# Optimization experiments

Measured on AMD Instinct MI355X. Metric: run time of the kernel, lower is better.

Reference implementation:

```python
import jax, jax.numpy as jnp
import numpy as np

ND, NP_, ED, EP, B = 8192, 8192, 262144, 262144, 4096
DIM = 300 + 1024 + 1024 + 1024  # 3372
EPS = 1e-5


def _bn(x, g, b):
    # BatchNorm1d in training mode: biased batch statistics
    m = x.mean(0)
    v = x.var(0)
    return (x - m) * jax.lax.rsqrt(v + EPS) * g + b


def _gcn(x, ei, ew, W, bias):
    # PyG GCNConv: add self-loops (weight 1), symmetric deg^-1/2 normalization,
    # linear transform, scatter-add aggregation at target nodes.
    N = x.shape[0]
    loop = jnp.arange(N)
    src = jnp.concatenate([ei[0], loop])
    dst = jnp.concatenate([ei[1], loop])
    w = jnp.concatenate([ew, jnp.ones((N,), ew.dtype)])
    deg = jax.ops.segment_sum(w, dst, num_segments=N)
    dinv = jnp.where(deg > 0, jax.lax.rsqrt(deg), 0.0)
    norm = dinv[src] * w * dinv[dst]          # [E+N]
    h = x @ W                                  # [N, 512]
    out = jax.ops.segment_sum(h[src] * norm[:, None], dst, num_segments=N) + bias
    return jax.nn.leaky_relu(out, 0.01)


def setup_inputs() -> dict:
    key = jax.random.key(0)
    ks = jax.random.split(key, 32)
    s = 0.02
    inp = {
        'd_index': jax.random.randint(ks[0], (B,), 0, ND),
        'p_index': jax.random.randint(ks[1], (B,), 0, NP_),
        'd_vecs': jax.random.normal(ks[2], (B, 300), jnp.float32),
        'p_embeddings': jax.random.normal(ks[3], (B, 1024), jnp.float32),
        'd_ecfps': jax.random.uniform(ks[4], (ND, 1024), jnp.float32),
        'd_ei': jax.random.randint(ks[5], (2, ED), 0, ND),
        'd_ew': jax.random.uniform(ks[6], (ED,), jnp.float32),
        'p_gos': jax.random.uniform(ks[7], (NP_, 1024), jnp.float32),
        'p_ei': jax.random.randint(ks[8], (2, EP), 0, NP_),
        'p_ew': jax.random.uniform(ks[9], (EP,), jnp.float32),
        'affinity': jax.random.uniform(ks[10], (ND, NP_), jnp.float32),
        # GCNConv params
        'W_e': jax.random.normal(ks[11], (1024, 512), jnp.float32) * s,
        'b_e': jnp.zeros((512,), jnp.float32),
        'W_g': jax.random.normal(ks[12], (1024, 512), jnp.float32) * s,
        'b_g': jnp.zeros((512,), jnp.float32),
        # lin1 / lin2
        'W1': jax.random.normal(ks[13], (512, 512), jnp.float32) * s,
        'b1': jnp.zeros((512,), jnp.float32),
        'W2': jax.random.normal(ks[14], (512, 512), jnp.float32) * s,
        'b2': jnp.zeros((512,), jnp.float32),
        # output MLP: 3372 -> 1024 -> 256 -> 1 with BN+ReLU (dropout = eval identity)
        'Wo1': jax.random.normal(ks[15], (DIM, 1024), jnp.float32) * s,
        'bo1': jnp.zeros((1024,), jnp.float32),
        'g1': jnp.ones((1024,), jnp.float32),
        'be1': jnp.zeros((1024,), jnp.float32),
        'Wo2': jax.random.normal(ks[16], (1024, 256), jnp.float32) * s,
        'bo2': jnp.zeros((256,), jnp.float32),
        'g2': jnp.ones((256,), jnp.float32),
        'be2': jnp.zeros((256,), jnp.float32),
        'Wo3': jax.random.normal(ks[17], (256, 1), jnp.float32) * s,
        'bo3': jnp.zeros((1,), jnp.float32),
    }
    return inp


def reference(d_index, p_index, d_vecs, p_embeddings, d_ecfps, d_ei, d_ew,
              p_gos, p_ei, p_ew, affinity,
              W_e, b_e, W_g, b_g, W1, b1, W2, b2,
              Wo1, bo1, g1, be1, Wo2, bo2, g2, be2, Wo3, bo3):
    ecfps = _gcn(d_ecfps, d_ei, d_ew, W_e, b_e)          # [ND, 512]
    gos = _gcn(p_gos, p_ei, p_ew, W_g, b_g)              # [NP, 512]
    drug = ecfps[d_index]                                 # [B, 512]
    protein = gos[p_index]                                # [B, 512]
    p2d = jax.nn.relu((affinity @ gos) @ W1 + b1)[d_index]      # [B, 512]
    d2p = jax.nn.relu((affinity.T @ ecfps) @ W2 + b2)[p_index]  # [B, 512]
    drug = jnp.concatenate([drug, p2d], axis=1)
    protein = jnp.concatenate([protein, d2p], axis=1)
    feature = jnp.concatenate([d_vecs, p_embeddings, drug, protein], axis=1)  # [B, 3372]
    h = jax.nn.relu(_bn(feature @ Wo1 + bo1, g1, be1))
    h = jax.nn.relu(_bn(h @ Wo2 + bo2, g2, be2))
    y = h @ Wo3 + bo3                                     # [B, 1]
    return y
```

## Files before the change

kernel.cpp:

```cpp
#include <hip/hip_runtime.h>
#include <stdint.h>
#include <stddef.h>

typedef unsigned short u16;
typedef unsigned int u32;
typedef __attribute__((ext_vector_type(8))) short bf16x8;
typedef __attribute__((ext_vector_type(8))) u16 u16x8;
typedef __attribute__((ext_vector_type(4))) float f32x4;

#define NDN 8192
#define NPN 8192
#define EDN 262144
#define EPN 262144
#define BBN 4096
#define KPAD 3392

__device__ __forceinline__ u16 f2b(float f) {
  u32 u = __float_as_uint(f);
  u32 r = (u + 0x7fffu + ((u >> 16) & 1u)) >> 16;
  return (u16)r;
}
__device__ __forceinline__ float b2f(u16 h) {
  return __uint_as_float(((u32)h) << 16);
}

__device__ __forceinline__ void gld_lds16(const void* g, void* l) {
  __builtin_amdgcn_global_load_lds(
      (const __attribute__((address_space(1))) u32*)g,
      (__attribute__((address_space(3))) u32*)l, 16, 0, 0);
}

template<int BM, int BN, int WM, int WN, bool GATHER>
__global__ void __launch_bounds__(256, 3)
gemm_bf16(const u16* __restrict__ A, int lda,
          const u16* __restrict__ Bt, int ldb,
          int N, int K, int KZ,
          const int* __restrict__ idx,
          float* __restrict__ Cf, u16* __restrict__ Cb, long zstride,
          const float* __restrict__ bias,
          const float* __restrict__ rowscale,
          int relu)
{
  constexpr int AISS = BM / 32;
  constexpr int BISS = BN / 32;
  constexpr int AF = WM / 16;
  constexpr int BF = WN / 16;
  constexpr int WGN = BN / WN;
  __shared__ __align__(16) u16 ldsA[BM * 64];
  __shared__ __align__(16) u16 ldsB[BN * 64];
  const int t = threadIdx.x;
  const int lane = t & 63;
  const int w = t >> 6;
  const int m0 = blockIdx.x * BM;
  const int n0 = blockIdx.y * BN;
  const int kOff = blockIdx.z * KZ;
  const int Kloc = min(KZ, K - kOff);
  const int wm = w / WGN, wn = w % WGN;
  const int sr = t >> 3;
  const int sk = (t & 7) * 8;

  if (zstride) Cf += (long)blockIdx.z * zstride;

  const u16* arow[AISS];
#pragma unroll
  for (int j = 0; j < AISS; ++j) {
    int r = m0 + j * 32 + sr;
    long rr = GATHER ? (long)idx[r] : (long)r;
    arow[j] = A + rr * (long)lda + sk + kOff;
  }
  const u16* brow[BISS];
#pragma unroll
  for (int j = 0; j < BISS; ++j)
    brow[j] = Bt + (long)(n0 + j * 32 + sr) * ldb + sk + kOff;

  f32x4 acc[AF][BF];
#pragma unroll
  for (int i = 0; i < AF; ++i)
#pragma unroll
    for (int j = 0; j < BF; ++j)
      acc[i][j] = (f32x4){0.f, 0.f, 0.f, 0.f};

  for (int k0 = 0; k0 < Kloc; k0 += 64) {
#pragma unroll
    for (int j = 0; j < AISS; ++j)
      gld_lds16(arow[j] + k0, &ldsA[(j * 32 + w * 8) * 64]);
#pragma unroll
    for (int j = 0; j < BISS; ++j)
      gld_lds16(brow[j] + k0, &ldsB[(j * 32 + w * 8) * 64]);
    __syncthreads();
#pragma unroll
    for (int k2 = 0; k2 < 64; k2 += 32) {
      bf16x8 af[AF], bfv[BF];
#pragma unroll
      for (int i = 0; i < AF; ++i)
        af[i] = *(const bf16x8*)&ldsA[(wm * WM + i * 16 + (lane & 15)) * 64 + k2 + (lane >> 4) * 8];
#pragma unroll
      for (int i = 0; i < BF; ++i)
        bfv[i] = *(const bf16x8*)&ldsB[(wn * WN + i * 16 + (lane & 15)) * 64 + k2 + (lane >> 4) * 8];
#pragma unroll
      for (int i = 0; i < AF; ++i)
#pragma unroll
        for (int j = 0; j < BF; ++j)
          acc[i][j] = __builtin_amdgcn_mfma_f32_16x16x32_bf16(af[i], bfv[j], acc[i][j], 0, 0, 0);
    }
    __syncthreads();
  }

  const int er = (lane >> 4) * 4;
  const int ecn = lane & 15;
#pragma unroll
  for (int i = 0; i < AF; ++i)
#pragma unroll
    for (int j = 0; j < BF; ++j)
#pragma unroll
      for (int r = 0; r < 4; ++r) {
        long gm = m0 + wm * WM + i * 16 + er + r;
        long gn = n0 + wn * WN + j * 16 + ecn;
        float v = acc[i][j][r];
        if (bias) v += bias[gn];
        if (rowscale) v *= rowscale[gm];
        if (relu) v = fmaxf(v, 0.f);
        if (Cb) Cb[gm * N + gn] = f2b(v);
        else    Cf[gm * N + gn] = v;
      }
}

__global__ void __launch_bounds__(256, 3)
gemm_a32g(const float* __restrict__ A, int lda,
          const u16* __restrict__ Bt, int ldb,
          int N, int KZ,
          const int* __restrict__ idx,
          float* __restrict__ Cf, long zstride)
{
  constexpr int AF = 2, BF = 8, WGN = 2;
  __shared__ __align__(16) u16 ldsA[64 * 72];
  __shared__ __align__(16) u16 ldsB[256 * 64];
  const int t = threadIdx.x;
  const int lane = t & 63;
  const int w = t >> 6;
  const int m0 = blockIdx.x * 64;
  const int n0 = blockIdx.y * 256;
  const int kOff = blockIdx.z * KZ;
  const int wm = w / WGN, wn = w % WGN;
  const int sr = t >> 3;
  const int sk = (t & 7) * 8;

  Cf += (long)blockIdx.z * zstride;

  const u16* brow[8];
#pragma unroll
  for (int j = 0; j < 8; ++j)
    brow[j] = Bt + (long)(n0 + j * 32 + sr) * ldb + sk + kOff;

  int r = m0 + (t >> 2);
  long rowsel = idx ? (long)idx[r] : (long)r;
  const float* ar_direct = A + rowsel * (long)lda + (t & 3) * 16 + kOff;

  f32x4 acc[AF][BF];
#pragma unroll
  for (int i = 0; i < AF; ++i)
#pragma unroll
    for (int j = 0; j < BF; ++j)
      acc[i][j] = (f32x4){0.f, 0.f, 0.f, 0.f};

  for (int k0 = 0; k0 < KZ; k0 += 64) {
#pragma unroll
    for (int j = 0; j < 8; ++j)
      gld_lds16(brow[j] + k0, &ldsB[(j * 32 + w * 8) * 64]);

    const float4* src = (const float4*)(ar_direct + k0);
    float4 v0 = src[0], v1 = src[1], v2 = src[2], v3 = src[3];
    u16x8 ua, ub;
    ua[0] = f2b(v0.x); ua[1] = f2b(v0.y); ua[2] = f2b(v0.z); ua[3] = f2b(v0.w);
    ua[4] = f2b(v1.x); ua[5] = f2b(v1.y); ua[6] = f2b(v1.z); ua[7] = f2b(v1.w);
    ub[0] = f2b(v2.x); ub[1] = f2b(v2.y); ub[2] = f2b(v2.z); ub[3] = f2b(v2.w);
    ub[4] = f2b(v3.x); ub[5] = f2b(v3.y); ub[6] = f2b(v3.z); ub[7] = f2b(v3.w);
    int ro = (t >> 2) * 72 + (t & 3) * 16;
    *(u16x8*)&ldsA[ro] = ua;
    *(u16x8*)&ldsA[ro + 8] = ub;
    __syncthreads();
#pragma unroll
    for (int k2 = 0; k2 < 64; k2 += 32) {
      bf16x8 af[AF], bfv[BF];
#pragma unroll
      for (int i = 0; i < AF; ++i)
        af[i] = *(const bf16x8*)&ldsA[(wm * 32 + i * 16 + (lane & 15)) * 72 + k2 + (lane >> 4) * 8];
#pragma unroll
      for (int i = 0; i < BF; ++i)
        bfv[i] = *(const bf16x8*)&ldsB[(wn * 128 + i * 16 + (lane & 15)) * 64 + k2 + (lane >> 4) * 8];
#pragma unroll
      for (int i = 0; i < AF; ++i)
#pragma unroll
        for (int j = 0; j < BF; ++j)
          acc[i][j] = __builtin_amdgcn_mfma_f32_16x16x32_bf16(af[i], bfv[j], acc[i][j], 0, 0, 0);
    }
    __syncthreads();
  }

  const int er = (lane >> 4) * 4;
  const int ecn = lane & 15;
#pragma unroll
  for (int i = 0; i < AF; ++i)
#pragma unroll
    for (int j = 0; j < BF; ++j)
#pragma unroll
      for (int rr2 = 0; rr2 < 4; ++rr2) {
        long gm = m0 + wm * 32 + i * 16 + er + rr2;
        long gn = n0 + wn * 128 + j * 16 + ecn;
        Cf[gm * N + gn] = acc[i][j][rr2];
      }
}

__global__ void reduceP(const float* __restrict__ p, long n, int parts,
                        int nmask, const float* __restrict__ bias,
                        float* __restrict__ out) {
  long i = ((long)blockIdx.x * 256 + threadIdx.x) * 4;
  if (i >= n) return;
  float4 a = *(const float4*)&p[i];
  for (int z = 1; z < parts; ++z) {
    float4 b = *(const float4*)&p[(long)z * n + i];
    a.x += b.x; a.y += b.y; a.z += b.z; a.w += b.w;
  }
  if (bias) {
    int c = (int)(i & nmask);
    a.x += bias[c]; a.y += bias[c + 1]; a.z += bias[c + 2]; a.w += bias[c + 3];
  }
  *(float4*)&out[i] = a;
}

__global__ void __launch_bounds__(256)
transcvt(const float* __restrict__ in, u16* __restrict__ out) {
  __shared__ float tile[64][65];
  const int t = threadIdx.x;
  const int r0 = blockIdx.x * 64, c0 = blockIdx.y * 64;
  {
    int rr = t >> 2, cb = (t & 3) * 16;
    const float4* src = (const float4*)&in[(long)(r0 + rr) * 8192 + c0 + cb];
    float4 a = src[0], b = src[1], c = src[2], d = src[3];
    float* dst = &tile[rr][cb];
    *(float4*)(dst) = a; *(float4*)(dst + 4) = b;
    *(float4*)(dst + 8) = c; *(float4*)(dst + 12) = d;
  }
  __syncthreads();
  {
    int cc = t >> 2, rb = (t & 3) * 16;
    u16x8 ua, ub;
#pragma unroll
    for (int j = 0; j < 8; ++j) {
      ua[j] = f2b(tile[rb + j][cc]);
      ub[j] = f2b(tile[rb + 8 + j][cc]);
    }
    u16* dst = &out[(long)(c0 + cc) * 8192 + r0 + rb];
    *(u16x8*)dst = ua;
    *(u16x8*)(dst + 8) = ub;
  }
}

__global__ void __launch_bounds__(256, 2)
gemm_sp(const float* __restrict__ A, int lda,
        const u16* __restrict__ Bt, int ldb,
        int N, int K,
        const float* __restrict__ bias,
        float* __restrict__ Cf)
{
  __shared__ __align__(16) u16 ldsAh[64 * 64];
  __shared__ __align__(16) u16 ldsAl[64 * 64];
  __shared__ __align__(16) u16 ldsB[64 * 64];
  const int t = threadIdx.x, lane = t & 63, w = t >> 6;
  const int m0 = blockIdx.x * 64, n0 = blockIdx.y * 64;
  const int wm = w >> 1, wn = w & 1;
  const int sr = t >> 3, sk = (t & 7) * 8;
  const int ar = t >> 2;
  const int ak = (t & 3) * 16;
  const float* Ap = A + (long)(m0 + ar) * lda + ak;
  const u16* brow[2];
#pragma unroll
  for (int j = 0; j < 2; ++j)
    brow[j] = Bt + (long)(n0 + j * 32 + sr) * ldb + sk;

  f32x4 acc[2][2];
#pragma unroll
  for (int i = 0; i < 2; ++i)
#pragma unroll
    for (int j = 0; j < 2; ++j)
      acc[i][j] = (f32x4){0.f, 0.f, 0.f, 0.f};

  for (int k0 = 0; k0 < K; k0 += 64) {
#pragma unroll
    for (int j = 0; j < 2; ++j)
      gld_lds16(brow[j] + k0, &ldsB[(j * 32 + w * 8) * 64]);
    const float4* src = (const float4*)(Ap + k0);
    float4 v0 = src[0], v1 = src[1], v2 = src[2], v3 = src[3];
    float f[16] = {v0.x, v0.y, v0.z, v0.w, v1.x, v1.y, v1.z, v1.w,
                   v2.x, v2.y, v2.z, v2.w, v3.x, v3.y, v3.z, v3.w};
    u16x8 h0, h1v, l0, l1v;
#pragma unroll
    for (int i = 0; i < 8; ++i) {
      u16 h = f2b(f[i]);       h0[i] = h;  l0[i] = f2b(f[i] - b2f(h));
      u16 g = f2b(f[8 + i]);   h1v[i] = g; l1v[i] = f2b(f[8 + i] - b2f(g));
    }
    *(u16x8*)&ldsAh[ar * 64 + ak] = h0;
    *(u16x8*)&ldsAh[ar * 64 + ak + 8] = h1v;
    *(u16x8*)&ldsAl[ar * 64 + ak] = l0;
    *(u16x8*)&ldsAl[ar * 64 + ak + 8] = l1v;
    __syncthreads();
#pragma unroll
    for (int k2 = 0; k2 < 64; k2 += 32) {
      bf16x8 ah[2], al[2], bv[2];
#pragma unroll
      for (int i = 0; i < 2; ++i) {
        int off = (wm * 32 + i * 16 + (lane & 15)) * 64 + k2 + (lane >> 4) * 8;
        ah[i] = *(const bf16x8*)&ldsAh[off];
        al[i] = *(const bf16x8*)&ldsAl[off];
      }
#pragma unroll
      for (int i = 0; i < 2; ++i)
        bv[i] = *(const bf16x8*)&ldsB[(wn * 32 + i * 16 + (lane & 15)) * 64 + k2 + (lane >> 4) * 8];
#pragma unroll
      for (int i = 0; i < 2; ++i)
#pragma unroll
        for (int j = 0; j < 2; ++j) {
          acc[i][j] = __builtin_amdgcn_mfma_f32_16x16x32_bf16(ah[i], bv[j], acc[i][j], 0, 0, 0);
          acc[i][j] = __builtin_amdgcn_mfma_f32_16x16x32_bf16(al[i], bv[j], acc[i][j], 0, 0, 0);
        }
    }
    __syncthreads();
  }

  const int er = (lane >> 4) * 4;
  const int ecn = lane & 15;
#pragma unroll
  for (int i = 0; i < 2; ++i)
#pragma unroll
    for (int j = 0; j < 2; ++j)
#pragma unroll
      for (int r = 0; r < 4; ++r) {
        long gm = m0 + wm * 32 + i * 16 + er + r;
        long gn = n0 + wn * 32 + j * 16 + ecn;
        float v = acc[i][j][r] + bias[gn];
        Cf[gm * N + gn] = fmaxf(v, 0.f);
      }
}

__global__ void cvt_bf16(const float* __restrict__ x, u16* __restrict__ y, long n) {
  long i = ((long)blockIdx.x * 256 + threadIdx.x) * 4;
  if (i < n) {
    float4 v = *(const float4*)&x[i];
    u16 a = f2b(v.x), b = f2b(v.y), c = f2b(v.z), d = f2b(v.w);
    u32 lo = (u32)a | ((u32)b << 16);
    u32 hi = (u32)c | ((u32)d << 16);
    *(uint2*)&y[i] = make_uint2(lo, hi);
  }
}

__global__ void wtrans(const float* __restrict__ in, u16* __restrict__ out,
                       int R, int C, int Rpad) {
  __shared__ float tile[32][33];
  int r0 = blockIdx.x * 32, c0 = blockIdx.y * 32;
  int tx = threadIdx.x & 31, ty = threadIdx.x >> 5;
  for (int j = 0; j < 32; j += 8) {
    int r = r0 + ty + j, c = c0 + tx;
    tile[ty + j][tx] = (r < R && c < C) ? in[(long)r * C + c] : 0.f;
  }
  __syncthreads();
  for (int j = 0; j < 32; j += 8) {
    int c = c0 + ty + j, r = r0 + tx;
    if (c < C && r < Rpad) out[(long)c * Rpad + r] = f2b(tile[tx][ty + j]);
  }
}

__global__ void btrans(const u16* __restrict__ in, u16* __restrict__ out, int R, int C) {
  __shared__ u16 tile[32][34];
  int r0 = blockIdx.x * 32, c0 = blockIdx.y * 32;
  int tx = threadIdx.x & 31, ty = threadIdx.x >> 5;
  for (int j = 0; j < 32; j += 8)
    tile[ty + j][tx] = in[(long)(r0 + ty + j) * C + c0 + tx];
  __syncthreads();
  for (int j = 0; j < 32; j += 8)
    out[(long)(c0 + ty + j) * R + r0 + tx] = tile[tx][ty + j];
}

__global__ void edge_deg2(const int* __restrict__ ei_a, const float* __restrict__ ew_a,
                          const int* __restrict__ ei_b, const float* __restrict__ ew_b,
                          int E, float* degw_a, int* cnt_a,
                          float* degw_b, int* cnt_b) {
  int e = blockIdx.x * 256 + threadIdx.x;
  if (e >= E) return;
  const int* ei = blockIdx.y ? ei_b : ei_a;
  const float* ew = blockIdx.y ? ew_b : ew_a;
  float* degw = blockIdx.y ? degw_b : degw_a;
  int* cnt = blockIdx.y ? cnt_b : cnt_a;
  int dst = ei[E + e];
  atomicAdd(&degw[dst], ew[e]);
  atomicAdd(&cnt[dst], 1);
}

__global__ void scan_dinv(const int* __restrict__ cnt_a, int* rowptr_a, int* cursor_a,
                          const float* __restrict__ degw_a, float* dinv_a,
                          const int* __restrict__ cnt_b, int* rowptr_b, int* cursor_b,
                          const float* __restrict__ degw_b, float* dinv_b) {
  const int* cnt = blockIdx.x ? cnt_b : cnt_a;
  int* rowptr = blockIdx.x ? rowptr_b : rowptr_a;
  int* cursor = blockIdx.x ? cursor_b : cursor_a;
  const float* degw = blockIdx.x ? degw_b : degw_a;
  float* dinv = blockIdx.x ? dinv_b : dinv_a;
  __shared__ int lds[256];
  int t = threadIdx.x;
  int c0 = t * 32;
  int loc[32];
  int s = 0;
#pragma unroll
  for (int i = 0; i < 32; ++i) { loc[i] = cnt[c0 + i]; s += loc[i]; }
  lds[t] = s;
  __syncthreads();
  for (int off = 1; off < 256; off <<= 1) {
    int add = (t >= off) ? lds[t - off] : 0;
    __syncthreads();
    lds[t] += add;
    __syncthreads();
  }
  int run = lds[t] - s;
#pragma unroll
  for (int i = 0; i < 32; ++i) {
    rowptr[c0 + i] = run;
    cursor[c0 + i] = run;
    run += loc[i];
  }
  if (t == 255) rowptr[8192] = run;
#pragma unroll
  for (int i = 0; i < 32; ++i)
    dinv[c0 + i] = rsqrtf(degw[c0 + i] + 1.0f);
}

__global__ void edge_scatter2(const int* __restrict__ ei_a, const float* __restrict__ ew_a,
                              const int* __restrict__ ei_b, const float* __restrict__ ew_b,
                              int E, int* cursor_a, int2* edges_a,
                              int* cursor_b, int2* edges_b) {
  int e = blockIdx.x * 256 + threadIdx.x;
  if (e >= E) return;
  const int* ei = blockIdx.y ? ei_b : ei_a;
  const float* ew = blockIdx.y ? ew_b : ew_a;
  int* cursor = blockIdx.y ? cursor_b : cursor_a;
  int2* edges = blockIdx.y ? edges_b : edges_a;
  int src = ei[e], dst = ei[E + e];
  int pos = atomicAdd(&cursor[dst], 1);
  edges[pos] = make_int2(src, __float_as_int(ew[e]));
}

__global__ void gcn_aggregate(const u16* __restrict__ hs,
                              const int* __restrict__ rowptr,
                              const int2* __restrict__ edges,
                              const float* __restrict__ dinv,
                              const float* __restrict__ bias,
                              u16* __restrict__ out) {
  const int i = blockIdx.x;
  const int t = threadIdx.x;
  const u32* base = (const u32*)hs;
  u32 hv = base[i * 256 + t];
  float a0 = b2f((u16)(hv & 0xffff));
  float a1 = b2f((u16)(hv >> 16));
  int s = rowptr[i], e = rowptr[i + 1];
  int p = s;
  for (; p + 4 <= e; p += 4) {
    int2 e0 = edges[p], e1 = edges[p + 1], e2 = edges[p + 2], e3 = edges[p + 3];
    u32 v0 = base[(long)e0.x * 256 + t];
    u32 v1 = base[(long)e1.x * 256 + t];
    u32 v2 = base[(long)e2.x * 256 + t];
    u32 v3 = base[(long)e3.x * 256 + t];
    float w0 = __int_as_float(e0.y), w1 = __int_as_float(e1.y);
    float w2 = __int_as_float(e2.y), w3 = __int_as_float(e3.y);
    a0 += w0 * b2f((u16)(v0 & 0xffff)); a1 += w0 * b2f((u16)(v0 >> 16));
    a0 += w1 * b2f((u16)(v1 & 0xffff)); a1 += w1 * b2f((u16)(v1 >> 16));
    a0 += w2 * b2f((u16)(v2 & 0xffff)); a1 += w2 * b2f((u16)(v2 >> 16));
    a0 += w3 * b2f((u16)(v3 & 0xffff)); a1 += w3 * b2f((u16)(v3 >> 16));
  }
  for (; p < e; ++p) {
    int2 ee = edges[p];
    u32 v = base[(long)ee.x * 256 + t];
    float ww = __int_as_float(ee.y);
    a0 += ww * b2f((u16)(v & 0xffff));
    a1 += ww * b2f((u16)(v >> 16));
  }
  float di = dinv[i];
  float o0 = bias[2 * t] + di * a0;
  float o1 = bias[2 * t + 1] + di * a1;
  o0 = (o0 >= 0.f) ? o0 : 0.01f * o0;
  o1 = (o1 >= 0.f) ? o1 : 0.01f * o1;
  ((u32*)out)[i * 256 + t] = (u32)f2b(o0) | ((u32)f2b(o1) << 16);
}

__global__ void colsum_all(const float* __restrict__ d_vecs, const float* __restrict__ p_emb,
                           const u16* __restrict__ ec, const u16* __restrict__ gos,
                           const float* __restrict__ t1, const float* __restrict__ t2,
                           const int* __restrict__ didx, const int* __restrict__ pidx,
                           float* __restrict__ out) {
  int c = blockIdx.x * 256 + threadIdx.x;
  if (c >= 3372) return;
  int r0 = blockIdx.y * 128;
  float s = 0.f;
  if (c < 300) {
    for (int r = r0; r < r0 + 128; ++r) s += d_vecs[(long)r * 300 + c];
  } else if (c < 1324) {
    int cc = c - 300;
    for (int r = r0; r < r0 + 128; ++r) s += p_emb[(long)r * 1024 + cc];
  } else if (c < 1836) {
    int cc = c - 1324;
    for (int r = r0; r < r0 + 128; ++r) s += b2f(ec[(long)didx[r] * 512 + cc]);
  } else if (c < 2348) {
    int cc = c - 1836;
    for (int r = r0; r < r0 + 128; ++r) s += t1[(long)r * 512 + cc];
  } else if (c < 2860) {
    int cc = c - 2348;
    for (int r = r0; r < r0 + 128; ++r) s += b2f(gos[(long)pidx[r] * 512 + cc]);
  } else {
    int cc = c - 2860;
    for (int r = r0; r < r0 + 128; ++r) s += t2[(long)r * 512 + cc];
  }
  atomicAdd(&out[c], s);
}

__global__ void assemble(const float* __restrict__ d_vecs, const float* __restrict__ p_emb,
                         const u16* __restrict__ ec, const u16* __restrict__ gos,
                         const float* __restrict__ t1, const float* __restrict__ t2,
                         const int* __restrict__ didx, const int* __restrict__ pidx,
                         const float* __restrict__ cs, u16* __restrict__ feat) {
  const float is = 1.f / 4096.f;
  int b = blockIdx.x;
  int t = threadIdx.x;
  long ob = (long)b * KPAD;
  int di = didx[b], pi = pidx[b];
  for (int j = t; j < 300; j += 256)
    feat[ob + j] = f2b(d_vecs[(long)b * 300 + j] - cs[j] * is);
  for (int j = t; j < 1024; j += 256)
    feat[ob + 300 + j] = f2b(p_emb[(long)b * 1024 + j] - cs[300 + j] * is);
  for (int j = t; j < 512; j += 256) {
    feat[ob + 1324 + j] = f2b(b2f(ec[(long)di * 512 + j]) - cs[1324 + j] * is);
    feat[ob + 1836 + j] = f2b(t1[(long)b * 512 + j] - cs[1836 + j] * is);
    feat[ob + 2348 + j] = f2b(b2f(gos[(long)pi * 512 + j]) - cs[2348 + j] * is);
    feat[ob + 2860 + j] = f2b(t2[(long)b * 512 + j] - cs[2860 + j] * is);
  }
  for (int j = t; j < 20; j += 256) feat[ob + 3372 + j] = 0;
}

__global__ void bn_stats(const float* __restrict__ x, int N,
                         float* __restrict__ sum, float* __restrict__ sumsq) {
  int r0 = blockIdx.x * 32;
  int t = threadIdx.x;
  for (int c = t; c < N; c += 256) {
    float s = 0.f, q = 0.f;
    for (int r = 0; r < 32; ++r) {
      float v = x[(long)(r0 + r) * N + c];
      s += v; q += v * v;
    }
    atomicAdd(&sum[c], s);
    atomicAdd(&sumsq[c], q);
  }
}

__global__ void bn_apply(const float* __restrict__ x, int M, int N, int nmask,
                         const float* __restrict__ sum, const float* __restrict__ sumsq,
                         const float* __restrict__ g, const float* __restrict__ be,
                         u16* __restrict__ y) {
  long i = (long)blockIdx.x * 256 + threadIdx.x;
  if (i >= (long)M * N) return;
  int c = (int)(i & nmask);
  float m = sum[c] / (float)M;
  float v = sumsq[c] / (float)M - m * m;
  float sc = g[c] * rsqrtf(v + 1e-5f);
  float sh = be[c] - m * sc;
  float o = fmaxf(x[i] * sc + sh, 0.f);
  y[i] = f2b(o);
}

__global__ void final_dot(const u16* __restrict__ h, const float* __restrict__ w,
                          const float* __restrict__ b0, float* __restrict__ y) {
  int wv = threadIdx.x >> 6, lane = threadIdx.x & 63;
  int row = blockIdx.x * 4 + wv;
  const u16* hr = h + (long)row * 256;
  ushort4 u = *(const ushort4*)&hr[lane * 4];
  float acc = b2f(u.x) * w[lane * 4] + b2f(u.y) * w[lane * 4 + 1] +
              b2f(u.z) * w[lane * 4 + 2] + b2f(u.w) * w[lane * 4 + 3];
  for (int off = 32; off; off >>= 1) acc += __shfl_down(acc, off);
  if (lane == 0) y[row] = acc + b0[0];
}

extern "C" void kernel_launch(void* const* d_in, const int* in_sizes, int n_in,
                              void* d_out, int out_size, void* d_ws, size_t ws_size,
                              hipStream_t stream) {
  (void)in_sizes; (void)n_in; (void)out_size; (void)ws_size;
  const int*   d_index  = (const int*)d_in[0];
  const int*   p_index  = (const int*)d_in[1];
  const float* d_vecs   = (const float*)d_in[2];
  const float* p_emb    = (const float*)d_in[3];
  const float* d_ecfps  = (const float*)d_in[4];
  const int*   d_ei     = (const int*)d_in[5];
  const float* d_ew     = (const float*)d_in[6];
  const float* p_gos    = (const float*)d_in[7];
  const int*   p_ei     = (const int*)d_in[8];
  const float* p_ew     = (const float*)d_in[9];
  const float* affinity = (const float*)d_in[10];
  const float* W_e  = (const float*)d_in[11];
  const float* b_e  = (const float*)d_in[12];
  const float* W_g  = (const float*)d_in[13];
  const float* b_g  = (const float*)d_in[14];
  const float* W1   = (const float*)d_in[15];
  const float* b1   = (const float*)d_in[16];
  const float* W2   = (const float*)d_in[17];
  const float* b2   = (const float*)d_in[18];
  const float* Wo1  = (const float*)d_in[19];
  const float* bo1  = (const float*)d_in[20];
  const float* g1   = (const float*)d_in[21];
  const float* be1  = (const float*)d_in[22];
  const float* Wo2  = (const float*)d_in[23];
  const float* bo2  = (const float*)d_in[24];
  const float* g2   = (const float*)d_in[25];
  const float* be2  = (const float*)d_in[26];
  const float* Wo3  = (const float*)d_in[27];
  const float* bo3  = (const float*)d_in[28];
  float* y_out = (float*)d_out;

  char* p = (char*)d_ws;
  auto alloc = [&](size_t bytes) -> char* {
    char* q = p;
    p += (bytes + 255) & ~(size_t)255;
    return q;
  };

  char* zero_start = p;
  float* degw_e = (float*)alloc(NDN * 4);
  int*   cnt_e  = (int*)alloc(NDN * 4);
  float* degw_p = (float*)alloc(NPN * 4);
  int*   cnt_p  = (int*)alloc(NPN * 4);
  float* bnsum1 = (float*)alloc(1024 * 4);
  float* bnsq1  = (float*)alloc(1024 * 4);
  float* bnsum2 = (float*)alloc(256 * 4);
  float* bnsq2  = (float*)alloc(256 * 4);
  float* colsum = (float*)alloc(KPAD * 4);
  size_t zero_bytes = (size_t)(p - zero_start);

  float* dinv_e   = (float*)alloc(NDN * 4);
  float* dinv_p   = (float*)alloc(NPN * 4);
  int*   rowptr_e = (int*)alloc((NDN + 1) * 4);
  int*   cursor_e = (int*)alloc(NDN * 4);
  int*   rowptr_p = (int*)alloc((NPN + 1) * 4);
  int*   cursor_p = (int*)alloc(NPN * 4);
  int2*  edges_e  = (int2*)alloc((size_t)EDN * 8);
  int2*  edges_p  = (int2*)alloc((size_t)EPN * 8);
  u16* x_e_b  = (u16*)alloc((size_t)NDN * 1024 * 2);
  u16* x_g_b  = (u16*)alloc((size_t)NPN * 1024 * 2);
  u16* WeT    = (u16*)alloc((size_t)512 * 1024 * 2);
  u16* WgT    = (u16*)alloc((size_t)512 * 1024 * 2);
  u16* W1T    = (u16*)alloc((size_t)512 * 512 * 2);
  u16* W2T    = (u16*)alloc((size_t)512 * 512 * 2);
  u16* Wo1T   = (u16*)alloc((size_t)1024 * KPAD * 2);
  u16* Wo2T   = (u16*)alloc((size_t)256 * 1024 * 2);
  u16* hs_e   = (u16*)alloc((size_t)NDN * 512 * 2);
  u16* hs_g   = (u16*)alloc((size_t)NPN * 512 * 2);
  u16* ec_b   = (u16*)alloc((size_t)NDN * 512 * 2);
  u16* gos_b  = (u16*)alloc((size_t)NPN * 512 * 2);
  u16* ecT_b  = (u16*)alloc((size_t)512 * NDN * 2);
  u16* gosT_b = (u16*)alloc((size_t)512 * NPN * 2);
  u16* affT_b = (u16*)alloc((size_t)8192 * 8192 * 2);
  u16* feat_b = (u16*)alloc((size_t)BBN * KPAD * 2);
  float* h1   = (float*)alloc((size_t)BBN * 1024 * 4);
  u16* h1n_b  = (u16*)alloc((size_t)BBN * 1024 * 2);
  float* h2   = (float*)alloc((size_t)BBN * 256 * 4);
  u16* h2n_b  = (u16*)alloc((size_t)BBN * 256 * 2);
  float* partK = (float*)alloc((size_t)4 * BBN * 512 * 4);

  float* tmp1_f = (float*)x_e_b;
  float* tmp2_f = (float*)x_g_b;
  float* t1_f   = (float*)hs_e;
  float* t2_f   = (float*)hs_g;

  hipMemsetAsync(zero_start, 0, zero_bytes, stream);

  cvt_bf16<<<8192, 256, 0, stream>>>(d_ecfps, x_e_b, (long)NDN * 1024);
  cvt_bf16<<<8192, 256, 0, stream>>>(p_gos, x_g_b, (long)NPN * 1024);
  wtrans<<<dim3(32, 16), 256, 0, stream>>>(W_e, WeT, 1024, 512, 1024);
  wtrans<<<dim3(32, 16), 256, 0, stream>>>(W_g, WgT, 1024, 512, 1024);
  wtrans<<<dim3(16, 16), 256, 0, stream>>>(W1, W1T, 512, 512, 512);
  wtrans<<<dim3(16, 16), 256, 0, stream>>>(W2, W2T, 512, 512, 512);
  wtrans<<<dim3(106, 32), 256, 0, stream>>>(Wo1, Wo1T, 3372, 1024, KPAD);
  wtrans<<<dim3(32, 8), 256, 0, stream>>>(Wo2, Wo2T, 1024, 256, 1024);

  transcvt<<<dim3(128, 128), 256, 0, stream>>>(affinity, affT_b);

  edge_deg2<<<dim3(EDN / 256, 2), 256, 0, stream>>>(d_ei, d_ew, p_ei, p_ew, EDN,
                                                    degw_e, cnt_e, degw_p, cnt_p);
  scan_dinv<<<2, 256, 0, stream>>>(cnt_e, rowptr_e, cursor_e, degw_e, dinv_e,
                                   cnt_p, rowptr_p, cursor_p, degw_p, dinv_p);
  edge_scatter2<<<dim3(EDN / 256, 2), 256, 0, stream>>>(d_ei, d_ew, p_ei, p_ew, EDN,
                                                        cursor_e, edges_e,
                                                        cursor_p, edges_p);

  gemm_bf16<64, 128, 32, 64, false><<<dim3(128, 4), 256, 0, stream>>>(
      x_e_b, 1024, WeT, 1024, 512, 1024, 1024, nullptr,
      (float*)nullptr, hs_e, 0, (const float*)nullptr, dinv_e, 0);
  gemm_bf16<64, 128, 32, 64, false><<<dim3(128, 4), 256, 0, stream>>>(
      x_g_b, 1024, WgT, 1024, 512, 1024, 1024, nullptr,
      (float*)nullptr, hs_g, 0, (const float*)nullptr, dinv_p, 0);

  gcn_aggregate<<<NDN, 256, 0, stream>>>(hs_e, rowptr_e, edges_e, dinv_e, b_e, ec_b);
  gcn_aggregate<<<NPN, 256, 0, stream>>>(hs_g, rowptr_p, edges_p, dinv_p, b_g, gos_b);

  btrans<<<dim3(256, 16), 256, 0, stream>>>(ec_b, ecT_b, NDN, 512);
  btrans<<<dim3(256, 16), 256, 0, stream>>>(gos_b, gosT_b, NPN, 512);

  gemm_a32g<<<dim3(64, 2, 4), 256, 0, stream>>>(
      affinity, 8192, gosT_b, 8192, 512, 2048, d_index, partK, (long)BBN * 512);
  reduceP<<<2048, 256, 0, stream>>>(partK, (long)BBN * 512, 4, 0, nullptr, tmp1_f);

  gemm_bf16<64, 128, 32, 64, true><<<dim3(64, 4, 2), 256, 0, stream>>>(
      affT_b, 8192, ecT_b, 8192, 512, 8192, 4096, p_index,
      partK, (u16*)nullptr, (long)BBN * 512,
      (const float*)nullptr, (const float*)nullptr, 0);
  reduceP<<<2048, 256, 0, stream>>>(partK, (long)BBN * 512, 2, 0, nullptr, tmp2_f);

  gemm_sp<<<dim3(64, 8), 256, 0, stream>>>(
      tmp1_f, 512, W1T, 512, 512, 512, b1, t1_f);
  gemm_sp<<<dim3(64, 8), 256, 0, stream>>>(
      tmp2_f, 512, W2T, 512, 512, 512, b2, t2_f);

  colsum_all<<<dim3(14, 32), 256, 0, stream>>>(d_vecs, p_emb, ec_b, gos_b,
                                               t1_f, t2_f, d_index, p_index, colsum);

  assemble<<<BBN, 256, 0, stream>>>(d_vecs, p_emb, ec_b, gos_b, t1_f, t2_f,
                                    d_index, p_index, colsum, feat_b);

  gemm_bf16<64, 128, 32, 64, false><<<dim3(64, 8, 2), 256, 0, stream>>>(
      feat_b, KPAD, Wo1T, KPAD, 1024, KPAD, 1728, nullptr,
      partK, (u16*)nullptr, (long)BBN * 1024,
      (const float*)nullptr, (const float*)nullptr, 0);
  reduceP<<<4096, 256, 0, stream>>>(partK, (long)BBN * 1024, 2, 1023, bo1, h1);
  bn_stats<<<128, 256, 0, stream>>>(h1, 1024, bnsum1, bnsq1);
  bn_apply<<<16384, 256, 0, stream>>>(h1, BBN, 1024, 1023, bnsum1, bnsq1, g1, be1, h1n_b);

  gemm_bf16<64, 64, 32, 32, false><<<dim3(64, 4), 256, 0, stream>>>(
      h1n_b, 1024, Wo2T, 1024, 256, 1024, 1024, nullptr,
      h2, (u16*)nullptr, 0, bo2, (const float*)nullptr, 0);
  bn_stats<<<128, 256, 0, stream>>>(h2, 256, bnsum2, bnsq2);
  bn_apply<<<4096, 256, 0, stream>>>(h2, BBN, 256, 255, bnsum2, bnsq2, g2, be2, h2n_b);

  final_dot<<<1024, 256, 0, stream>>>(h2n_b, Wo3, bo3, y_out);
}
```

Measured before the change: 1.123 ms.

## Batch paired launches and fuse reduction, BN stats and final dot kernels

```diff
diff --git a/kernel.cpp b/kernel.cpp
--- a/kernel.cpp
+++ b/kernel.cpp
@@ -126,6 +126,83 @@
 }
 
 __global__ void __launch_bounds__(256, 3)
+gemm_dual(const u16* __restrict__ A0, const u16* __restrict__ A1, int lda,
+          const u16* __restrict__ B0, const u16* __restrict__ B1, int ldb,
+          int N, int K,
+          const float* __restrict__ rs0, const float* __restrict__ rs1,
+          u16* __restrict__ C0, u16* __restrict__ C1)
+{
+  const u16* A = blockIdx.z ? A1 : A0;
+  const u16* Bt = blockIdx.z ? B1 : B0;
+  const float* rowscale = blockIdx.z ? rs1 : rs0;
+  u16* Cb = blockIdx.z ? C1 : C0;
+  __shared__ __align__(16) u16 ldsA[64 * 64];
+  __shared__ __align__(16) u16 ldsB[128 * 64];
+  const int t = threadIdx.x;
+  const int lane = t & 63;
+  const int w = t >> 6;
+  const int m0 = blockIdx.x * 64;
+  const int n0 = blockIdx.y * 128;
+  const int wm = w / 2, wn = w % 2;
+  const int sr = t >> 3, sk = (t & 7) * 8;
+
+  const u16* arow[2];
+#pragma unroll
+  for (int j = 0; j < 2; ++j)
+    arow[j] = A + (long)(m0 + j * 32 + sr) * lda + sk;
+  const u16* brow[4];
+#pragma unroll
+  for (int j = 0; j < 4; ++j)
+    brow[j] = Bt + (long)(n0 + j * 32 + sr) * ldb + sk;
+
+  f32x4 acc[2][4];
+#pragma unroll
+  for (int i = 0; i < 2; ++i)
+#pragma unroll
+    for (int j = 0; j < 4; ++j)
+      acc[i][j] = (f32x4){0.f, 0.f, 0.f, 0.f};
+
+  for (int k0 = 0; k0 < K; k0 += 64) {
+#pragma unroll
+    for (int j = 0; j < 2; ++j)
+      gld_lds16(arow[j] + k0, &ldsA[(j * 32 + w * 8) * 64]);
+#pragma unroll
+    for (int j = 0; j < 4; ++j)
+      gld_lds16(brow[j] + k0, &ldsB[(j * 32 + w * 8) * 64]);
+    __syncthreads();
+#pragma unroll
+    for (int k2 = 0; k2 < 64; k2 += 32) {
+      bf16x8 af[2], bfv[4];
+#pragma unroll
+      for (int i = 0; i < 2; ++i)
+        af[i] = *(const bf16x8*)&ldsA[(wm * 32 + i * 16 + (lane & 15)) * 64 + k2 + (lane >> 4) * 8];
+#pragma unroll
+      for (int i = 0; i < 4; ++i)
+        bfv[i] = *(const bf16x8*)&ldsB[(wn * 64 + i * 16 + (lane & 15)) * 64 + k2 + (lane >> 4) * 8];
+#pragma unroll
+      for (int i = 0; i < 2; ++i)
+#pragma unroll
+        for (int j = 0; j < 4; ++j)
+          acc[i][j] = __builtin_amdgcn_mfma_f32_16x16x32_bf16(af[i], bfv[j], acc[i][j], 0, 0, 0);
+    }
+    __syncthreads();
+  }
+
+  const int er = (lane >> 4) * 4;
+  const int ecn = lane & 15;
+#pragma unroll
+  for (int i = 0; i < 2; ++i)
+#pragma unroll
+    for (int j = 0; j < 4; ++j)
+#pragma unroll
+      for (int r = 0; r < 4; ++r) {
+        long gm = m0 + wm * 32 + i * 16 + er + r;
+        long gn = n0 + wn * 64 + j * 16 + ecn;
+        Cb[gm * N + gn] = f2b(acc[i][j][r] * rowscale[gm]);
+      }
+}
+
+__global__ void __launch_bounds__(256, 3)
 gemm_a32g(const float* __restrict__ A, int lda,
           const u16* __restrict__ Bt, int ldb,
           int N, int KZ,
@@ -211,21 +288,41 @@
       }
 }
 
-__global__ void reduceP(const float* __restrict__ p, long n, int parts,
-                        int nmask, const float* __restrict__ bias,
-                        float* __restrict__ out) {
+__global__ void reduce_both(const float* __restrict__ p1, const float* __restrict__ p2,
+                            long n, float* __restrict__ o1, float* __restrict__ o2) {
   long i = ((long)blockIdx.x * 256 + threadIdx.x) * 4;
   if (i >= n) return;
-  float4 a = *(const float4*)&p[i];
-  for (int z = 1; z < parts; ++z) {
-    float4 b = *(const float4*)&p[(long)z * n + i];
+  if (blockIdx.z == 0) {
+    float4 a = *(const float4*)&p1[i];
+    for (int z = 1; z < 4; ++z) {
+      float4 b = *(const float4*)&p1[(long)z * n + i];
+      a.x += b.x; a.y += b.y; a.z += b.z; a.w += b.w;
+    }
+    *(float4*)&o1[i] = a;
+  } else {
+    float4 a = *(const float4*)&p2[i];
+    float4 b = *(const float4*)&p2[n + i];
     a.x += b.x; a.y += b.y; a.z += b.z; a.w += b.w;
-  }
-  if (bias) {
-    int c = (int)(i & nmask);
-    a.x += bias[c]; a.y += bias[c + 1]; a.z += bias[c + 2]; a.w += bias[c + 3];
-  }
-  *(float4*)&out[i] = a;
+    *(float4*)&o2[i] = a;
+  }
+}
+
+__global__ void reduce_h1_stats(const float* __restrict__ p, const float* __restrict__ bias,
+                                float* __restrict__ h1,
+                                float* __restrict__ sum, float* __restrict__ sq) {
+  int c = blockIdx.x * 256 + threadIdx.x;
+  int r0 = blockIdx.y * 64;
+  const long n = (long)BBN * 1024;
+  float b = bias[c];
+  float s = 0.f, q = 0.f;
+  for (int r = r0; r < r0 + 64; ++r) {
+    long o = (long)r * 1024 + c;
+    float v = p[o] + p[n + o] + b;
+    h1[o] = v;
+    s += v; q += v * v;
+  }
+  atomicAdd(&sum[c], s);
+  atomicAdd(&sq[c], q);
 }
 
 __global__ void __launch_bounds__(256)
@@ -256,13 +353,17 @@
   }
 }
 
-__global__ void __launch_bounds__(256, 2)
-gemm_sp(const float* __restrict__ A, int lda,
-        const u16* __restrict__ Bt, int ldb,
-        int N, int K,
-        const float* __restrict__ bias,
-        float* __restrict__ Cf)
+__global__ void __launch_bounds__(256, 3)
+gemm_sp2(const float* __restrict__ A0, const float* __restrict__ A1, int lda,
+         const u16* __restrict__ B0, const u16* __restrict__ B1, int ldb,
+         int N, int K,
+         const float* __restrict__ b0p, const float* __restrict__ b1p,
+         float* __restrict__ C0, float* __restrict__ C1)
 {
+  const float* A = blockIdx.z ? A1 : A0;
+  const u16* Bt = blockIdx.z ? B1 : B0;
+  const float* bias = blockIdx.z ? b1p : b0p;
+  float* Cf = blockIdx.z ? C1 : C0;
   __shared__ __align__(16) u16 ldsAh[64 * 64];
   __shared__ __align__(16) u16 ldsAl[64 * 64];
   __shared__ __align__(16) u16 ldsB[64 * 64];
@@ -342,34 +443,48 @@
       }
 }
 
-__global__ void cvt_bf16(const float* __restrict__ x, u16* __restrict__ y, long n) {
+__global__ void cvt2(const float* __restrict__ x0, u16* __restrict__ y0,
+                     const float* __restrict__ x1, u16* __restrict__ y1, long n) {
+  const float* x = blockIdx.z ? x1 : x0;
+  u16* y = blockIdx.z ? y1 : y0;
   long i = ((long)blockIdx.x * 256 + threadIdx.x) * 4;
   if (i < n) {
     float4 v = *(const float4*)&x[i];
     u16 a = f2b(v.x), b = f2b(v.y), c = f2b(v.z), d = f2b(v.w);
-    u32 lo = (u32)a | ((u32)b << 16);
-    u32 hi = (u32)c | ((u32)d << 16);
-    *(uint2*)&y[i] = make_uint2(lo, hi);
-  }
-}
-
-__global__ void wtrans(const float* __restrict__ in, u16* __restrict__ out,
-                       int R, int C, int Rpad) {
+    *(uint2*)&y[i] = make_uint2((u32)a | ((u32)b << 16), (u32)c | ((u32)d << 16));
+  }
+}
+
+struct WtSeg { const float* in; u16* out; int R, C, Rpad, base, tx; };
+__global__ void wtrans_all(WtSeg s0, WtSeg s1, WtSeg s2, WtSeg s3, WtSeg s4, WtSeg s5) {
   __shared__ float tile[32][33];
-  int r0 = blockIdx.x * 32, c0 = blockIdx.y * 32;
+  WtSeg s;
+  int b = blockIdx.x;
+  if      (b >= s5.base) s = s5;
+  else if (b >= s4.base) s = s4;
+  else if (b >= s3.base) s = s3;
+  else if (b >= s2.base) s = s2;
+  else if (b >= s1.base) s = s1;
+  else                   s = s0;
+  int rel = b - s.base;
+  int r0 = (rel % s.tx) * 32, c0 = (rel / s.tx) * 32;
   int tx = threadIdx.x & 31, ty = threadIdx.x >> 5;
   for (int j = 0; j < 32; j += 8) {
     int r = r0 + ty + j, c = c0 + tx;
-    tile[ty + j][tx] = (r < R && c < C) ? in[(long)r * C + c] : 0.f;
+    tile[ty + j][tx] = (r < s.R && c < s.C) ? s.in[(long)r * s.C + c] : 0.f;
   }
   __syncthreads();
   for (int j = 0; j < 32; j += 8) {
     int c = c0 + ty + j, r = r0 + tx;
-    if (c < C && r < Rpad) out[(long)c * Rpad + r] = f2b(tile[tx][ty + j]);
-  }
-}
-
-__global__ void btrans(const u16* __restrict__ in, u16* __restrict__ out, int R, int C) {
+    if (c < s.C && r < s.Rpad) s.out[(long)c * s.Rpad + r] = f2b(tile[tx][ty + j]);
+  }
+}
+
+__global__ void btrans2(const u16* __restrict__ i0, u16* __restrict__ o0,
+                        const u16* __restrict__ i1, u16* __restrict__ o1,
+                        int R, int C) {
+  const u16* in = blockIdx.z ? i1 : i0;
+  u16* out = blockIdx.z ? o1 : o0;
   __shared__ u16 tile[32][34];
   int r0 = blockIdx.x * 32, c0 = blockIdx.y * 32;
   int tx = threadIdx.x & 31, ty = threadIdx.x >> 5;
@@ -447,13 +562,20 @@
   edges[pos] = make_int2(src, __float_as_int(ew[e]));
 }
 
-__global__ void gcn_aggregate(const u16* __restrict__ hs,
-                              const int* __restrict__ rowptr,
-                              const int2* __restrict__ edges,
-                              const float* __restrict__ dinv,
-                              const float* __restrict__ bias,
-                              u16* __restrict__ out) {
-  const int i = blockIdx.x;
+__global__ void agg2(const u16* __restrict__ hs_a, const int* __restrict__ rp_a,
+                     const int2* __restrict__ ed_a, const float* __restrict__ di_a,
+                     const float* __restrict__ bi_a, u16* __restrict__ out_a,
+                     const u16* __restrict__ hs_b, const int* __restrict__ rp_b,
+                     const int2* __restrict__ ed_b, const float* __restrict__ di_b,
+                     const float* __restrict__ bi_b, u16* __restrict__ out_b) {
+  const int gsel = blockIdx.x >> 13;
+  const int i = blockIdx.x & 8191;
+  const u16* hs = gsel ? hs_b : hs_a;
+  const int* rowptr = gsel ? rp_b : rp_a;
+  const int2* edges = gsel ? ed_b : ed_a;
+  const float* dinv = gsel ? di_b : di_a;
+  const float* bias = gsel ? bi_b : bi_a;
+  u16* out = gsel ? out_b : out_a;
   const int t = threadIdx.x;
   const u32* base = (const u32*)hs;
   u32 hv = base[i * 256 + t];
@@ -557,31 +679,51 @@
   }
 }
 
-__global__ void bn_apply(const float* __restrict__ x, int M, int N, int nmask,
-                         const float* __restrict__ sum, const float* __restrict__ sumsq,
+__global__ void bn_apply4(const float* __restrict__ x, int M, long total, int nmask,
+                          const float* __restrict__ sum, const float* __restrict__ sumsq,
+                          const float* __restrict__ g, const float* __restrict__ be,
+                          u16* __restrict__ y) {
+  long i = ((long)blockIdx.x * 256 + threadIdx.x) * 4;
+  if (i >= total) return;
+  float4 v = *(const float4*)&x[i];
+  int c = (int)(i & nmask);
+  float Mi = 1.f / (float)M;
+  u16 o[4];
+  float vv[4] = {v.x, v.y, v.z, v.w};
+#pragma unroll
+  for (int j = 0; j < 4; ++j) {
+    float m = sum[c + j] * Mi;
+    float var = sumsq[c + j] * Mi - m * m;
+    float sc = g[c + j] * rsqrtf(var + 1e-5f);
+    float sh = be[c + j] - m * sc;
+    o[j] = f2b(fmaxf(vv[j] * sc + sh, 0.f));
+  }
+  *(uint2*)&y[i] = make_uint2((u32)o[0] | ((u32)o[1] << 16), (u32)o[2] | ((u32)o[3] << 16));
+}
+
+__global__ void bn_final(const float* __restrict__ h2,
+                         const float* __restrict__ sum, const float* __restrict__ sq,
                          const float* __restrict__ g, const float* __restrict__ be,
-                         u16* __restrict__ y) {
-  long i = (long)blockIdx.x * 256 + threadIdx.x;
-  if (i >= (long)M * N) return;
-  int c = (int)(i & nmask);
-  float m = sum[c] / (float)M;
-  float v = sumsq[c] / (float)M - m * m;
-  float sc = g[c] * rsqrtf(v + 1e-5f);
-  float sh = be[c] - m * sc;
-  float o = fmaxf(x[i] * sc + sh, 0.f);
-  y[i] = f2b(o);
-}
-
-__global__ void final_dot(const u16* __restrict__ h, const float* __restrict__ w,
-                          const float* __restrict__ b0, float* __restrict__ y) {
+                         const float* __restrict__ w3, const float* __restrict__ b3,
+                         float* __restrict__ y) {
   int wv = threadIdx.x >> 6, lane = threadIdx.x & 63;
   int row = blockIdx.x * 4 + wv;
-  const u16* hr = h + (long)row * 256;
-  ushort4 u = *(const ushort4*)&hr[lane * 4];
-  float acc = b2f(u.x) * w[lane * 4] + b2f(u.y) * w[lane * 4 + 1] +
-              b2f(u.z) * w[lane * 4 + 2] + b2f(u.w) * w[lane * 4 + 3];
+  float4 v = *(const float4*)&h2[(long)row * 256 + lane * 4];
+  float vv[4] = {v.x, v.y, v.z, v.w};
+  const float Mi = 1.f / 4096.f;
+  float acc = 0.f;
+#pragma unroll
+  for (int j = 0; j < 4; ++j) {
+    int c = lane * 4 + j;
+    float m = sum[c] * Mi;
+    float var = sq[c] * Mi - m * m;
+    float sc = g[c] * rsqrtf(var + 1e-5f);
+    float sh = be[c] - m * sc;
+    float h = fmaxf(vv[j] * sc + sh, 0.f);
+    acc += h * w3[c];
+  }
   for (int off = 32; off; off >>= 1) acc += __shfl_down(acc, off);
-  if (lane == 0) y[row] = acc + b0[0];
+  if (lane == 0) y[row] = acc + b3[0];
 }
 
 extern "C" void kernel_launch(void* const* d_in, const int* in_sizes, int n_in,
@@ -665,8 +807,8 @@
   float* h1   = (float*)alloc((size_t)BBN * 1024 * 4);
   u16* h1n_b  = (u16*)alloc((size_t)BBN * 1024 * 2);
   float* h2   = (float*)alloc((size_t)BBN * 256 * 4);
-  u16* h2n_b  = (u16*)alloc((size_t)BBN * 256 * 2);
-  float* partK = (float*)alloc((size_t)4 * BBN * 512 * 4);
+  float* partK  = (float*)alloc((size_t)4 * BBN * 512 * 4);
+  float* partK2 = (float*)alloc((size_t)2 * BBN * 512 * 4);
 
   float* tmp1_f = (float*)x_e_b;
   float* tmp2_f = (float*)x_g_b;
@@ -675,15 +817,16 @@
 
   hipMemsetAsync(zero_start, 0, zero_bytes, stream);
 
-  cvt_bf16<<<8192, 256, 0, stream>>>(d_ecfps, x_e_b, (long)NDN * 1024);
-  cvt_bf16<<<8192, 256, 0, stream>>>(p_gos, x_g_b, (long)NPN * 1024);
-  wtrans<<<dim3(32, 16), 256, 0, stream>>>(W_e, WeT, 1024, 512, 1024);
-  wtrans<<<dim3(32, 16), 256, 0, stream>>>(W_g, WgT, 1024, 512, 1024);
-  wtrans<<<dim3(16, 16), 256, 0, stream>>>(W1, W1T, 512, 512, 512);
-  wtrans<<<dim3(16, 16), 256, 0, stream>>>(W2, W2T, 512, 512, 512);
-  wtrans<<<dim3(106, 32), 256, 0, stream>>>(Wo1, Wo1T, 3372, 1024, KPAD);
-  wtrans<<<dim3(32, 8), 256, 0, stream>>>(Wo2, Wo2T, 1024, 256, 1024);
-
+  cvt2<<<dim3(8192, 1, 2), 256, 0, stream>>>(d_ecfps, x_e_b, p_gos, x_g_b, (long)NDN * 1024);
+  {
+    WtSeg s0{W_e,  WeT,  1024, 512,  1024, 0,                         32};
+    WtSeg s1{W_g,  WgT,  1024, 512,  1024, 512,                       32};
+    WtSeg s2{W1,   W1T,  512,  512,  512,  1024,                      16};
+    WtSeg s3{W2,   W2T,  512,  512,  512,  1280,                      16};
+    WtSeg s4{Wo1,  Wo1T, 3372, 1024, KPAD, 1536,                      106};
+    WtSeg s5{Wo2,  Wo2T, 1024, 256,  1024, 1536 + 3392,               32};
+    wtrans_all<<<1536 + 3392 + 256, 256, 0, stream>>>(s0, s1, s2, s3, s4, s5);
+  }
   transcvt<<<dim3(128, 128), 256, 0, stream>>>(affinity, affT_b);
 
   edge_deg2<<<dim3(EDN / 256, 2), 256, 0, stream>>>(d_ei, d_ew, p_ei, p_ew, EDN,
@@ -694,37 +837,29 @@
                                                         cursor_e, edges_e,
                                                         cursor_p, edges_p);
 
-  gemm_bf16<64, 128, 32, 64, false><<<dim3(128, 4), 256, 0, stream>>>(
-      x_e_b, 1024, WeT, 1024, 512, 1024, 1024, nullptr,
-      (float*)nullptr, hs_e, 0, (const float*)nullptr, dinv_e, 0);
-  gemm_bf16<64, 128, 32, 64, false><<<dim3(128, 4), 256, 0, stream>>>(
-      x_g_b, 1024, WgT, 1024, 512, 1024, 1024, nullptr,
-      (float*)nullptr, hs_g, 0, (const float*)nullptr, dinv_p, 0);
-
-  gcn_aggregate<<<NDN, 256, 0, stream>>>(hs_e, rowptr_e, edges_e, dinv_e, b_e, ec_b);
-  gcn_aggregate<<<NPN, 256, 0, stream>>>(hs_g, rowptr_p, edges_p, dinv_p, b_g, gos_b);
-
-  btrans<<<dim3(256, 16), 256, 0, stream>>>(ec_b, ecT_b, NDN, 512);
-  btrans<<<dim3(256, 16), 256, 0, stream>>>(gos_b, gosT_b, NPN, 512);
+  gemm_dual<<<dim3(128, 4, 2), 256, 0, stream>>>(
+      x_e_b, x_g_b, 1024, WeT, WgT, 1024, 512, 1024,
+      dinv_e, dinv_p, hs_e, hs_g);
+
+  agg2<<<16384, 256, 0, stream>>>(hs_e, rowptr_e, edges_e, dinv_e, b_e, ec_b,
+                                  hs_g, rowptr_p, edges_p, dinv_p, b_g, gos_b);
+
+  btrans2<<<dim3(256, 16, 2), 256, 0, stream>>>(ec_b, ecT_b, gos_b, gosT_b, NDN, 512);
 
   gemm_a32g<<<dim3(64, 2, 4), 256, 0, stream>>>(
       affinity, 8192, gosT_b, 8192, 512, 2048, d_index, partK, (long)BBN * 512);
-  reduceP<<<2048, 256, 0, stream>>>(partK, (long)BBN * 512, 4, 0, nullptr, tmp1_f);
-
   gemm_bf16<64, 128, 32, 64, true><<<dim3(64, 4, 2), 256, 0, stream>>>(
       affT_b, 8192, ecT_b, 8192, 512, 8192, 4096, p_index,
-      partK, (u16*)nullptr, (long)BBN * 512,
+      partK2, (u16*)nullptr, (long)BBN * 512,
       (const float*)nullptr, (const float*)nullptr, 0);
-  reduceP<<<2048, 256, 0, stream>>>(partK, (long)BBN * 512, 2, 0, nullptr, tmp2_f);
-
-  gemm_sp<<<dim3(64, 8), 256, 0, stream>>>(
-      tmp1_f, 512, W1T, 512, 512, 512, b1, t1_f);
-  gemm_sp<<<dim3(64, 8), 256, 0, stream>>>(
-      tmp2_f, 512, W2T, 512, 512, 512, b2, t2_f);
+  reduce_both<<<dim3(2048, 1, 2), 256, 0, stream>>>(partK, partK2, (long)BBN * 512,
+                                                    tmp1_f, tmp2_f);
+
+  gemm_sp2<<<dim3(64, 8, 2), 256, 0, stream>>>(
+      tmp1_f, tmp2_f, 512, W1T, W2T, 512, 512, 512, b1, b2, t1_f, t2_f);
 
   colsum_all<<<dim3(14, 32), 256, 0, stream>>>(d_vecs, p_emb, ec_b, gos_b,
                                                t1_f, t2_f, d_index, p_index, colsum);
-
   assemble<<<BBN, 256, 0, stream>>>(d_vecs, p_emb, ec_b, gos_b, t1_f, t2_f,
                                     d_index, p_index, colsum, feat_b);
 
@@ -732,15 +867,14 @@
       feat_b, KPAD, Wo1T, KPAD, 1024, KPAD, 1728, nullptr,
       partK, (u16*)nullptr, (long)BBN * 1024,
       (const float*)nullptr, (const float*)nullptr, 0);
-  reduceP<<<4096, 256, 0, stream>>>(partK, (long)BBN * 1024, 2, 1023, bo1, h1);
-  bn_stats<<<128, 256, 0, stream>>>(h1, 1024, bnsum1, bnsq1);
-  bn_apply<<<16384, 256, 0, stream>>>(h1, BBN, 1024, 1023, bnsum1, bnsq1, g1, be1, h1n_b);
+  reduce_h1_stats<<<dim3(4, 64), 256, 0, stream>>>(partK, bo1, h1, bnsum1, bnsq1);
+  bn_apply4<<<4096, 256, 0, stream>>>(h1, BBN, (long)BBN * 1024, 1023,
+                                      bnsum1, bnsq1, g1, be1, h1n_b);
 
   gemm_bf16<64, 64, 32, 32, false><<<dim3(64, 4), 256, 0, stream>>>(
       h1n_b, 1024, Wo2T, 1024, 256, 1024, 1024, nullptr,
       h2, (u16*)nullptr, 0, bo2, (const float*)nullptr, 0);
   bn_stats<<<128, 256, 0, stream>>>(h2, 256, bnsum2, bnsq2);
-  bn_apply<<<4096, 256, 0, stream>>>(h2, BBN, 256, 255, bnsum2, bnsq2, g2, be2, h2n_b);
-
-  final_dot<<<1024, 256, 0, stream>>>(h2n_b, Wo3, bo3, y_out);
-}
+
+  bn_final<<<1024, 256, 0, stream>>>(h2, bnsum2, bnsq2, g2, be2, Wo3, bo3, y_out);
+}
```

After: 1.046 ms. 6.8% less time.
